# Kernel tuning notes

Measured on AMD Instinct MI355X. Metric: run time of the kernel, lower is better.

The kernel has to match this reference:

```python
import jax, jax.numpy as jnp
import numpy as np

N, E = 20000, 640000
D_IN, D_H, D_OUT = 128, 64, 32


def _lin_w(key, out_d, in_d):
    return jax.random.normal(key, (out_d, in_d), jnp.float32) / np.sqrt(in_d)


def setup_inputs() -> dict:
    key = jax.random.key(0)
    ks = jax.random.split(key, 16)
    x = jax.random.normal(ks[0], (N, D_IN), jnp.float32)
    edge_index = jax.random.randint(ks[1], (2, E), 0, N, jnp.int64)
    inp = {"x": x, "edge_index": edge_index}
    # SAGEConv weights: lin_l (aggregated neighbors, with bias), lin_r (root, no bias)
    inp["Wl1"] = _lin_w(ks[2], D_H, D_IN); inp["bl1"] = jnp.zeros((D_H,), jnp.float32)
    inp["Wr1"] = _lin_w(ks[3], D_H, D_IN)
    inp["Wl2"] = _lin_w(ks[4], D_H, D_H); inp["bl2"] = jnp.zeros((D_H,), jnp.float32)
    inp["Wr2"] = _lin_w(ks[5], D_H, D_H)
    inp["Wl3"] = _lin_w(ks[6], D_OUT, D_H); inp["bl3"] = jnp.zeros((D_OUT,), jnp.float32)
    inp["Wr3"] = _lin_w(ks[7], D_OUT, D_H)
    # Conv2d kernels (OIHW), all 3x3 pad 1
    inp["Wc1"] = jax.random.normal(ks[8], (D_H, 1, 3, 3), jnp.float32) / 3.0
    inp["bc1"] = jnp.zeros((D_H,), jnp.float32)
    inp["Wc2"] = jax.random.normal(ks[9], (D_H, D_H, 3, 3), jnp.float32) / np.sqrt(9 * D_H)
    inp["bc2"] = jnp.zeros((D_H,), jnp.float32)
    inp["Wc3"] = jax.random.normal(ks[10], (1, D_H, 3, 3), jnp.float32) / np.sqrt(9 * D_H)
    inp["bc3"] = jnp.zeros((1,), jnp.float32)
    # linear2 (hidden -> hidden)
    inp["W2"] = _lin_w(ks[11], D_H, D_H); inp["b2"] = jnp.zeros((D_H,), jnp.float32)
    return inp


def _sage(x, src, dst, Wl, bl, Wr):
    # PyG SAGEConv (mean aggr): lin_l(mean_{j->i} x_j) + lin_r(x_i)
    msg = x[src]  # [E, d] gather
    agg = jax.ops.segment_sum(msg, dst, num_segments=N)
    deg = jax.ops.segment_sum(jnp.ones((src.shape[0], 1), x.dtype), dst, num_segments=N)
    agg = agg / jnp.maximum(deg, 1.0)
    return agg @ Wl.T + bl + x @ Wr.T


def _conv(x, w, b):
    y = jax.lax.conv_general_dilated(x, w, (1, 1), ((1, 1), (1, 1)),
                                     dimension_numbers=("NCHW", "OIHW", "NCHW"))
    return y + b[None, :, None, None]


def reference(x, edge_index, Wl1, bl1, Wr1, Wl2, bl2, Wr2, Wl3, bl3, Wr3,
              Wc1, bc1, Wc2, bc2, Wc3, bc3, W2, b2):
    src, dst = edge_index[0], edge_index[1]
    h = _sage(x, src, dst, Wl1, bl1, Wr1)
    h = _sage(h, src, dst, Wl2, bl2, Wr2)
    h = _sage(h, src, dst, Wl2, bl2, Wr2)  # sage2 reused, as in source
    out_1 = h
    h4 = h[None, None]                     # [1,1,N,D_H]
    out = _conv(h4, Wc1, bc1)              # [1,D_H,N,D_H]
    out = _conv(out, Wc2, bc2)             # dropout is identity at inference
    out = _conv(out, Wc3, bc3)             # [1,1,N,D_H]
    out = out[0, 0] + out_1
    out = out @ W2.T + b2
    h = _sage(out, src, dst, Wl2, bl2, Wr2)
    h = _sage(h, src, dst, Wl2, bl2, Wr2)
    h = _sage(h, src, dst, Wl3, bl3, Wr3)
    return h
```

## Files before the change

### kernel.cpp

```cpp
#include <hip/hip_runtime.h>

#define NN 20000
#define NE 640000
#define NBUK 79

__device__ __forceinline__ int probe_stride(const int* __restrict__ ei32) {
  int lane = threadIdx.x & 63;
  int v = ei32[2 * lane + 1];
  unsigned long long nz = __ballot(v != 0);
  return (nz == 0ull) ? 2 : 1;
}

__global__ __launch_bounds__(256) void k_histB(const int* __restrict__ ei,
                                               int* __restrict__ bins, int E) {
  __shared__ int lb[NBUK];
  int tid = threadIdx.x;
  int st = probe_stride(ei);
  for (int i = tid; i < NBUK; i += 256) lb[i] = 0;
  __syncthreads();
  int e0 = blockIdx.x * 4096;
#pragma unroll
  for (int t = 0; t < 16; ++t) {
    int e = e0 + t * 256 + tid;
    if (e < E) atomicAdd(&lb[ei[(size_t)(E + e) * st] >> 8], 1);
  }
  __syncthreads();
  for (int i = tid; i < NBUK; i += 256)
    if (lb[i]) atomicAdd(&bins[i], lb[i]);
}

__global__ __launch_bounds__(128) void k_scan79(const int* __restrict__ bins,
                                                int* __restrict__ bbase,
                                                int* __restrict__ bcur,
                                                int* __restrict__ rowptr,
                                                int E, int N) {
  __shared__ int lds[128];
  int tid = threadIdx.x;
  int mine = (tid < NBUK) ? bins[tid] : 0;
  lds[tid] = mine;
  __syncthreads();
  for (int off = 1; off < 128; off <<= 1) {
    int v = (tid >= off) ? lds[tid - off] : 0;
    __syncthreads();
    lds[tid] += v;
    __syncthreads();
  }
  int ex = lds[tid] - mine;
  if (tid <= NBUK) {
    bbase[tid] = ex;
    if (tid < NBUK) bcur[tid] = ex;
  }
  if (tid == 0) rowptr[N] = E;
}

__global__ __launch_bounds__(256) void k_part(const int* __restrict__ ei,
                                              int* __restrict__ bcur,
                                              unsigned long long* __restrict__ ebuf,
                                              int E) {
  __shared__ int lcnt[NBUK];
  __shared__ int lbase[NBUK];
  int tid = threadIdx.x;
  int st = probe_stride(ei);
  for (int i = tid; i < NBUK; i += 256) lcnt[i] = 0;
  __syncthreads();
  int e0 = blockIdx.x * 4096;
  int srcv[16], dstv[16], lrank[16], bk[16];
  int n = 0;
#pragma unroll
  for (int t = 0; t < 16; ++t) {
    int e = e0 + t * 256 + tid;
    if (e < E) {
      int s = ei[(size_t)e * st];
      int d = ei[(size_t)(E + e) * st];
      int b = d >> 8;
      srcv[n] = s; dstv[n] = d; bk[n] = b;
      lrank[n] = atomicAdd(&lcnt[b], 1);
      ++n;
    }
  }
  __syncthreads();
  for (int i = tid; i < NBUK; i += 256)
    lbase[i] = atomicAdd(&bcur[i], lcnt[i]);
  __syncthreads();
  for (int t = 0; t < n; ++t) {
    int pos = lbase[bk[t]] + lrank[t];
    ebuf[pos] = ((unsigned long long)(unsigned)dstv[t] << 32) | (unsigned)srcv[t];
  }
}

__global__ __launch_bounds__(256) void k_sortb(
    const unsigned long long* __restrict__ ebuf, const int* __restrict__ bbase,
    int* __restrict__ rowptr, float* __restrict__ invdeg,
    int* __restrict__ csr, int N) {
  __shared__ int lcnt[256];
  __shared__ int lcur[256];
  __shared__ int wsum[4];
  int b = blockIdx.x;
  int tid = threadIdx.x;
  int base = bbase[b], n = bbase[b + 1] - base;
  lcnt[tid] = 0;
  __syncthreads();
  for (int e = tid; e < n; e += 256) {
    int d = (int)(ebuf[base + e] >> 32);
    atomicAdd(&lcnt[d - (b << 8)], 1);
  }
  __syncthreads();
  int c = lcnt[tid];
  int lane = tid & 63, wid = tid >> 6;
  int s = c;
#pragma unroll
  for (int off = 1; off < 64; off <<= 1) {
    int v = __shfl_up(s, off, 64);
    if (lane >= off) s += v;
  }
  if (lane == 63) wsum[wid] = s;
  __syncthreads();
  int woff = 0;
  for (int w = 0; w < wid; ++w) woff += wsum[w];
  int pref = woff + s - c;
  int gnode = (b << 8) + tid;
  if (gnode < N) {
    rowptr[gnode] = base + pref;
    invdeg[gnode] = 1.0f / (float)(c < 1 ? 1 : c);
  }
  lcur[tid] = pref;
  __syncthreads();
  for (int e = tid; e < n; e += 256) {
    unsigned long long pk = ebuf[base + e];
    int d = (int)(pk >> 32);
    int pos = atomicAdd(&lcur[d - (b << 8)], 1);
    csr[base + pos] = (int)(unsigned)pk;
  }
}

__device__ __forceinline__ bool maskB(int var, int o2, int o1) {
  int s = o2 + o1;
  switch (var) {
    case 0: return (o2 >= 0) && (s >= 0);
    case 1: return s >= -1;
    case 3: return s <= 1;
    case 4: return (o2 <= 0) && (s <= 0);
    default: return true;
  }
}

__global__ __launch_bounds__(256) void k_setup2(
    const float* __restrict__ Wc1, const float* __restrict__ Wc2,
    const float* __restrict__ Wc3, const float* __restrict__ bc1,
    const float* __restrict__ bc2, const float* __restrict__ bc3,
    const float* __restrict__ Wl1, const float* __restrict__ Wr1,
    const float* __restrict__ Wl2, const float* __restrict__ Wr2,
    const float* __restrict__ Wl3, const float* __restrict__ Wr3,
    const float* __restrict__ W2, const float* __restrict__ b2,
    const float* __restrict__ bl2,
    float* __restrict__ T729, float* __restrict__ beta5,
    float* __restrict__ Wf, float* __restrict__ bf,
    float* __restrict__ Wt1, float* __restrict__ Wt2,
    float* __restrict__ Wt3, float* __restrict__ W2t,
    float* __restrict__ Sbuf, float* __restrict__ c5) {
  int b = blockIdx.x, tid = threadIdx.x;
  if (b == 0) {
    __shared__ float W3[576];
    __shared__ float S9s[5184];
    __shared__ float W1s[576];
    for (int e = tid; e < 576; e += 256) { W3[e] = Wc3[e]; W1s[e] = Wc1[e]; }
    __syncthreads();
    for (int bb = tid; bb < 576; bb += 256) {
      float acc[9];
#pragma unroll
      for (int a = 0; a < 9; ++a) acc[a] = 0.0f;
#pragma unroll 4
      for (int o = 0; o < 64; ++o) {
        float w2 = Wc2[o * 576 + bb];
#pragma unroll
        for (int a = 0; a < 9; ++a) acc[a] += W3[o * 9 + a] * w2;
      }
#pragma unroll
      for (int a = 0; a < 9; ++a) S9s[a * 576 + bb] = acc[a];
    }
    __syncthreads();
    for (int c = tid; c < 729; c += 256) {
      int kx0  = c % 3;
      int dl1e = (c / 3) % 3;
      int dl2e = (c / 9) % 3;
      int ky0  = (c / 27) % 3;
      int ky1  = (c / 81) % 3;
      int ky2  = c / 243;
      const float* s9 = &S9s[(ky2 * 3 + dl2e) * 576 + ky1 * 3 + dl1e];
      const float* w1 = &W1s[ky0 * 3 + kx0];
      float t = 0.0f;
#pragma unroll 8
      for (int i = 0; i < 64; ++i) t += s9[i * 9] * w1[i * 9];
      T729[c] = t;
    }
  } else if (b <= 5) {
    __shared__ float S2[576];
    __shared__ float W3b[576];
    __shared__ float B2[64];
    __shared__ float part[256];
    int var = b - 1;
    for (int e = tid; e < 576; e += 256) {
      int o = e / 9, r = e - o * 9;
      float t = 0.0f;
      for (int i = 0; i < 64; ++i) t += Wc2[o * 576 + i * 9 + r] * bc1[i];
      S2[e] = t;
      W3b[e] = Wc3[e];
    }
    if (tid < 64) B2[tid] = bc2[tid];
    __syncthreads();
    int u = tid & 63, oc = tid >> 6;
    float s = 0.0f;
    for (int ky2 = 0; ky2 < 3; ++ky2) {
      int o2 = ky2 - 1;
      bool okA = (var == 0) ? (o2 >= 0) : (var == 4) ? (o2 <= 0) : true;
      if (!okA) continue;
      for (int dl2 = -1; dl2 <= 1; ++dl2) {
        int p = u + dl2; if ((unsigned)p >= 64u) continue;
        float sel[9];
#pragma unroll
        for (int ky1 = 0; ky1 < 3; ++ky1) {
          int o1 = ky1 - 1;
          bool mb = maskB(var, o2, o1);
#pragma unroll
          for (int dl1 = -1; dl1 <= 1; ++dl1) {
            int pq = p + dl1;
            sel[ky1 * 3 + dl1 + 1] = (mb && (unsigned)pq < 64u) ? 1.0f : 0.0f;
          }
        }
#pragma unroll 4
        for (int oo = 0; oo < 16; ++oo) {
          int o = oc * 16 + oo;
          float inner = B2[o];
#pragma unroll
          for (int r = 0; r < 9; ++r) inner += S2[o * 9 + r] * sel[r];
          s += W3b[o * 9 + ky2 * 3 + (dl2 + 1)] * inner;
        }
      }
    }
    part[tid] = s;
    __syncthreads();
    if (tid < 64) {
      beta5[var * 64 + tid] =
          bc3[0] + part[tid] + part[64 + tid] + part[128 + tid] + part[192 + tid];
    }
  } else if (b <= 38) {
    int gidx = (b - 6) * 256 + tid;
    if (gidx < 8192) {
      int w = gidx >> 7, u = gidx & 127;
      const float* wsrc = (u < 64) ? &Wl2[u * 64] : &Wr2[(u - 64) * 64];
      float s = 0.0f;
#pragma unroll 4
      for (int k = 0; k < 64; ++k) s += W2[k * 64 + w] * wsrc[k];
      Wf[gidx] = s;
    } else if (gidx < 8320) {
      int u = gidx - 8192;
      const float* wsrc = (u < 64) ? &Wl2[u * 64] : &Wr2[(u - 64) * 64];
      float s = 0.0f;
#pragma unroll 4
      for (int k = 0; k < 64; ++k) s += b2[k] * wsrc[k];
      bf[u] = s;
    }
  } else {
    int idx = (b - 39) * 256 + tid;
    if (idx < 16384) {
      int w = idx >> 7, u = idx & 127;
      Wt1[idx] = (u < 64) ? Wl1[u * 128 + w] : Wr1[(u - 64) * 128 + w];
    } else if (idx < 24576) {
      int t = idx - 16384;
      int w = t >> 7, u = t & 127;
      Wt2[t] = (u < 64) ? Wl2[u * 64 + w] : Wr2[(u - 64) * 64 + w];
    } else if (idx < 28672) {
      int t = idx - 24576;
      int w = t >> 6, u = t & 63;
      Wt3[t] = (u < 32) ? Wl3[u * 64 + w] : Wr3[(u - 32) * 64 + w];
    } else if (idx < 32768) {
      int t = idx - 28672;
      int w = t >> 6, u = t & 63;
      W2t[t] = W2[u * 64 + w];
    } else if (idx < 45056) {
      int t2 = idx - 32768;
      int m = t2 >> 12, e = t2 & 4095;
      int i = e >> 6, j = e & 63;
      float s = 0.0f;
#pragma unroll 4
      for (int k = 0; k < 64; ++k) {
        float wlj = Wl2[j * 64 + k], wrj = Wr2[j * 64 + k];
        float wli = Wl2[k * 64 + i], wri = Wr2[k * 64 + i];
        if (m == 0) s += wli * wlj;
        else if (m == 1) s += wri * wlj + wli * wrj;
        else s += wri * wrj;
      }
      Sbuf[t2] = s;
    } else if (idx < 45120) {
      int j = idx - 45056;
      float s = bl2[j];
      for (int i = 0; i < 64; ++i)
        s += bl2[i] * (Wl2[j * 64 + i] + Wr2[j * 64 + i]);
      c5[j] = s;
    }
  }
}

__global__ __launch_bounds__(256) void k_setupG(
    const float* __restrict__ Sbuf, const float* __restrict__ c5,
    const float* __restrict__ Wl3, const float* __restrict__ Wr3,
    const float* __restrict__ bl3, float* __restrict__ Gbuf,
    float* __restrict__ c32) {
  int b = blockIdx.x, tid = threadIdx.x;
  if (b < 32) {
    int idx = b * 256 + tid;
    int kblk = idx >> 11;
    int rem = idx & 2047;
    int t = rem >> 5, j = rem & 31;
    const float* S2p = Sbuf;
    const float* S1p = Sbuf + 4096;
    const float* S0p = Sbuf + 8192;
    const float* pa = (kblk == 0) ? S2p : (kblk == 1) ? S1p : (kblk == 2) ? S0p : nullptr;
    const float* pb = (kblk == 1) ? S2p : (kblk == 2) ? S1p : (kblk == 3) ? S0p : nullptr;
    float s = 0.0f;
#pragma unroll 4
    for (int k = 0; k < 64; ++k) {
      if (pa) s += pa[t * 64 + k] * Wl3[j * 64 + k];
      if (pb) s += pb[t * 64 + k] * Wr3[j * 64 + k];
    }
    Gbuf[idx] = s;
  } else if (tid < 32) {
    float s = bl3[tid];
    for (int k = 0; k < 64; ++k)
      s += c5[k] * (Wl3[tid * 64 + k] + Wr3[tid * 64 + k]);
    c32[tid] = s;
  }
}

__global__ __launch_bounds__(256) void k_setupWg(
    const float* __restrict__ Gbuf, const float* __restrict__ W2,
    const float* __restrict__ b2, float* __restrict__ Wg,
    float* __restrict__ bg) {
  int b = blockIdx.x, tid = threadIdx.x;
  if (b < 32) {
    int idx = b * 256 + tid;
    int w = idx >> 7, u = idx & 127;
    int kblk = u >> 5, j = u & 31;
    const float* gp = Gbuf + kblk * 2048 + j;
    float s = 0.0f;
#pragma unroll 4
    for (int t = 0; t < 64; ++t) s += W2[t * 64 + w] * gp[t * 32];
    Wg[idx] = s;
  } else if (tid < 128) {
    int kblk = tid >> 5, j = tid & 31;
    const float* gp = Gbuf + kblk * 2048 + j;
    float s = 0.0f;
    for (int t = 0; t < 64; ++t) s += b2[t] * gp[t * 32];
    bg[tid] = s;
  }
}

__global__ __launch_bounds__(256) void k_m5(const float* __restrict__ T729,
                                            float* __restrict__ M5T) {
  __shared__ float Ts[729];
  int tid = threadIdx.x;
  for (int e = tid; e < 729; e += 256) Ts[e] = T729[e];
  __syncthreads();
  int idx = blockIdx.x * 256 + tid;
  if (idx >= 15680) return;
  int jw = idx % 7;
  int u  = (idx / 7) % 64;
  int d  = (idx / 448) % 7;
  int var = idx / 3136;
  int w = u + jw - 3;
  float s = 0.0f;
  if (w >= 0 && w < 64) {
    for (int ky2 = 0; ky2 < 3; ++ky2) {
      int o2 = ky2 - 1;
      for (int ky1 = 0; ky1 < 3; ++ky1) {
        int o1 = ky1 - 1;
        if (!maskB(var, o2, o1)) continue;
        int o0 = (d - 3) - o2 - o1;
        if (o0 < -1 || o0 > 1) continue;
        int ky0 = o0 + 1;
        int cbase = ((ky2 * 3 + ky1) * 3 + ky0) * 27;
#pragma unroll
        for (int kx0 = 0; kx0 < 3; ++kx0) {
          int jq = jw - kx0;
          if ((unsigned)jq >= 5u) continue;
          int q = u + jq - 2;
          if ((unsigned)q >= 64u) continue;
#pragma unroll
          for (int dl2e = 0; dl2e < 3; ++dl2e) {
            int p = u + dl2e - 1;
            if ((unsigned)p >= 64u) continue;
            int dl1e = jq - dl2e;
            if ((unsigned)dl1e >= 3u) continue;
            s += Ts[cbase + dl2e * 9 + dl1e * 3 + kx0];
          }
        }
      }
    }
  }
  if (d == 3 && jw == 3) s += 1.0f;
  M5T[(var * 49 + d * 7 + jw) * 64 + u] = s;
}

template <int C, int K>
__global__ __launch_bounds__(256) void k_gemm(const float* __restrict__ X,
                                              const float* __restrict__ Wt,
                                              const float* __restrict__ bias,
                                              float* __restrict__ out, int N) {
  constexpr int ROWS = 16;
  constexpr int RPT = ROWS * C / 256;
  __shared__ float Xs[ROWS * K];
  int y0 = blockIdx.x * ROWS;
  {
    const float4* src = (const float4*)(X + (size_t)y0 * K);
    float4* dst = (float4*)Xs;
#pragma unroll
    for (int v = 0; v < ROWS * K / 4 / 256; ++v)
      dst[v * 256 + threadIdx.x] = src[v * 256 + threadIdx.x];
  }
  __syncthreads();
  int u = threadIdx.x % C;
  int rg = threadIdx.x / C;
  float acc[RPT];
  float bv = bias ? bias[u] : 0.0f;
#pragma unroll
  for (int k = 0; k < RPT; ++k) acc[k] = bv;
#pragma unroll 2
  for (int w0 = 0; w0 < K; w0 += 4) {
    float m0 = Wt[(w0 + 0) * C + u];
    float m1 = Wt[(w0 + 1) * C + u];
    float m2 = Wt[(w0 + 2) * C + u];
    float m3 = Wt[(w0 + 3) * C + u];
    const float* xs = &Xs[(rg * RPT) * K + w0];
#pragma unroll
    for (int k = 0; k < RPT; ++k) {
      float4 h = *(const float4*)(xs + k * K);
      acc[k] += m0 * h.x + m1 * h.y + m2 * h.z + m3 * h.w;
    }
  }
#pragma unroll
  for (int k = 0; k < RPT; ++k)
    out[(size_t)(y0 + rg * RPT + k) * C + u] = acc[k];
}

template <int C>
__global__ __launch_bounds__(256) void k_fused(const float* __restrict__ yzin,
                                               const int* __restrict__ csr,
                                               const int* __restrict__ rowptr,
                                               const float* __restrict__ invdeg,
                                               const float* __restrict__ bl,
                                               const float* __restrict__ Wt,
                                               float* __restrict__ out, int N) {
  constexpr int FV = 16;
  constexpr int G  = 4;
  constexpr int S4 = 32;
  constexpr int CAP = 64;
  __shared__ int idxs[16 * CAP];
  __shared__ float htile[16 * 64];
  int tid = threadIdx.x;
  int w = tid >> 6, lane = tid & 63;
  int base = blockIdx.x * 16;
  int beg_r[4], m_r[4], end_r[4];
#pragma unroll
  for (int rr = 0; rr < 4; ++rr) {
    int node = base + w * 4 + rr;
    int beg = rowptr[node], end = rowptr[node + 1];
    beg_r[rr] = beg; end_r[rr] = end;
    int cnt = end - beg;
    int m = cnt < CAP ? cnt : CAP;
    m_r[rr] = m;
    int* my = &idxs[(w * 4 + rr) * CAP];
    for (int k = lane; k < m; k += 64) my[k] = csr[beg + k];
  }
  __syncthreads();
  int g = lane / FV, f = lane % FV;
  const float4* yz4 = (const float4*)yzin;
#pragma unroll
  for (int rr = 0; rr < 4; ++rr) {
    int node = base + w * 4 + rr;
    const int* my = &idxs[(w * 4 + rr) * CAP];
    int m = m_r[rr];
    float a0x=0,a0y=0,a0z=0,a0w=0, a1x=0,a1y=0,a1z=0,a1w=0;
    float a2x=0,a2y=0,a2z=0,a2w=0, a3x=0,a3y=0,a3z=0,a3w=0;
    int j = g;
    for (; j + 3 * G < m; j += 4 * G) {
      int s0 = my[j], s1 = my[j + G], s2 = my[j + 2 * G], s3 = my[j + 3 * G];
      float4 v0 = yz4[(size_t)s0 * S4 + f];
      float4 v1 = yz4[(size_t)s1 * S4 + f];
      float4 v2 = yz4[(size_t)s2 * S4 + f];
      float4 v3 = yz4[(size_t)s3 * S4 + f];
      a0x += v0.x; a0y += v0.y; a0z += v0.z; a0w += v0.w;
      a1x += v1.x; a1y += v1.y; a1z += v1.z; a1w += v1.w;
      a2x += v2.x; a2y += v2.y; a2z += v2.z; a2w += v2.w;
      a3x += v3.x; a3y += v3.y; a3z += v3.z; a3w += v3.w;
    }
    for (; j < m; j += G) {
      int s0 = my[j];
      float4 v0 = yz4[(size_t)s0 * S4 + f];
      a0x += v0.x; a0y += v0.y; a0z += v0.z; a0w += v0.w;
    }
    for (int jj = beg_r[rr] + CAP + g; jj < end_r[rr]; jj += G) {
      int s0 = csr[jj];
      float4 v0 = yz4[(size_t)s0 * S4 + f];
      a0x += v0.x; a0y += v0.y; a0z += v0.z; a0w += v0.w;
    }
    float ax = (a0x + a1x) + (a2x + a3x);
    float ay = (a0y + a1y) + (a2y + a3y);
    float az = (a0z + a1z) + (a2z + a3z);
    float aw = (a0w + a1w) + (a2w + a3w);
#pragma unroll
    for (int mm = FV; mm < 64; mm <<= 1) {
      ax += __shfl_xor(ax, mm, 64);
      ay += __shfl_xor(ay, mm, 64);
      az += __shfl_xor(az, mm, 64);
      aw += __shfl_xor(aw, mm, 64);
    }
    if (g == 0) {
      float4 root = yz4[(size_t)node * S4 + FV + f];
      float4 bv = ((const float4*)bl)[f];
      float id = invdeg[node];
      float4 o;
      o.x = ax * id + bv.x + root.x;
      o.y = ay * id + bv.y + root.y;
      o.z = az * id + bv.z + root.z;
      o.w = aw * id + bv.w + root.w;
// ... 201 lines not shown
  float a0x=0,a0y=0,a0z=0,a0w=0, a1x=0,a1y=0,a1z=0,a1w=0;
  float a2x=0,a2y=0,a2z=0,a2w=0, a3x=0,a3y=0,a3z=0,a3w=0;
  int j = g;
  for (; j + 3 * G < m; j += 4 * G) {
    int s0 = my[j], s1 = my[j + G], s2 = my[j + 2 * G], s3 = my[j + 3 * G];
    float4 v0 = sr4[(size_t)s0 * FV + f];
    float4 v1 = sr4[(size_t)s1 * FV + f];
    float4 v2 = sr4[(size_t)s2 * FV + f];
    float4 v3 = sr4[(size_t)s3 * FV + f];
    a0x += v0.x; a0y += v0.y; a0z += v0.z; a0w += v0.w;
    a1x += v1.x; a1y += v1.y; a1z += v1.z; a1w += v1.w;
    a2x += v2.x; a2y += v2.y; a2z += v2.z; a2w += v2.w;
    a3x += v3.x; a3y += v3.y; a3z += v3.z; a3w += v3.w;
  }
  for (; j < m; j += G) {
    int s0 = my[j];
    float4 v0 = sr4[(size_t)s0 * FV + f];
    a0x += v0.x; a0y += v0.y; a0z += v0.z; a0w += v0.w;
  }
  for (int jj = beg + CAP + g; jj < end; jj += G) {
    int s0 = csr[jj];
    float4 v0 = sr4[(size_t)s0 * FV + f];
    a0x += v0.x; a0y += v0.y; a0z += v0.z; a0w += v0.w;
  }
  float ax = (a0x + a1x) + (a2x + a3x);
  float ay = (a0y + a1y) + (a2y + a3y);
  float az = (a0z + a1z) + (a2z + a3z);
  float aw = (a0w + a1w) + (a2w + a3w);
#pragma unroll
  for (int mm = FV; mm < 64; mm <<= 1) {
    ax += __shfl_xor(ax, mm, 64);
    ay += __shfl_xor(ay, mm, 64);
    az += __shfl_xor(az, mm, 64);
    aw += __shfl_xor(aw, mm, 64);
  }
  if (g == 0) {
    float4 av = ((const float4*)add)[(size_t)node * FV + f];
    float id = invdeg[node];
    float4 o;
    o.x = ax * id + av.x;
    o.y = ay * id + av.y;
    o.z = az * id + av.z;
    o.w = aw * id + av.w;
    if (cvec != nullptr) {
      float4 cv = ((const float4*)cvec)[f];
      o.x += cv.x; o.y += cv.y; o.z += cv.z; o.w += cv.w;
    }
    ((float4*)out)[(size_t)node * FV + f] = o;
  }
}

extern "C" void kernel_launch(void* const* d_in, const int* in_sizes, int n_in,
                              void* d_out, int out_size, void* d_ws, size_t ws_size,
                              hipStream_t stream) {
  const int N = NN, E = NE;
  const float* x   = (const float*)d_in[0];
  const int*   ei  = (const int*)d_in[1];
  const float* Wl1 = (const float*)d_in[2];
  const float* bl1 = (const float*)d_in[3];
  const float* Wr1 = (const float*)d_in[4];
  const float* Wl2 = (const float*)d_in[5];
  const float* bl2 = (const float*)d_in[6];
  const float* Wr2 = (const float*)d_in[7];
  const float* Wl3 = (const float*)d_in[8];
  const float* bl3 = (const float*)d_in[9];
  const float* Wr3 = (const float*)d_in[10];
  const float* Wc1 = (const float*)d_in[11];
  const float* bc1 = (const float*)d_in[12];
  const float* Wc2 = (const float*)d_in[13];
  const float* bc2 = (const float*)d_in[14];
  const float* Wc3 = (const float*)d_in[15];
  const float* bc3 = (const float*)d_in[16];
  const float* W2  = (const float*)d_in[17];
  const float* b2  = (const float*)d_in[18];

  char* ws = (char*)d_ws;
  size_t off = 0;
  auto alloc = [&](size_t bytes) -> void* {
    off = (off + 255) & ~(size_t)255;
    void* p = ws + off;
    off += bytes;
    return p;
  };
  int*   rowptr = (int*)alloc((size_t)(N + 1) * 4);
  float* invdeg = (float*)alloc((size_t)N * 4);
  int*   csr    = (int*)alloc((size_t)E * 4);
  unsigned long long* ebuf = (unsigned long long*)alloc((size_t)E * 8);
  int*   bins   = (int*)alloc(128 * 4);
  int*   bbase  = (int*)alloc(128 * 4);
  int*   bcur   = (int*)alloc(128 * 4);
  float* Wt1    = (float*)alloc(128 * 128 * 4);
  float* Wt2    = (float*)alloc(64 * 128 * 4);
  float* Wt3    = (float*)alloc(64 * 64 * 4);
  float* W2t    = (float*)alloc(64 * 64 * 4);
  float* Wf     = (float*)alloc(64 * 128 * 4);
  float* bf     = (float*)alloc(128 * 4);
  float* T729   = (float*)alloc(729 * 4);
  float* M5T    = (float*)alloc(15680 * 4);
  float* beta5  = (float*)alloc(320 * 4);
  float* Sbuf   = (float*)alloc(12288 * 4);
  float* c5     = (float*)alloc(64 * 4);
  float* Gbuf   = (float*)alloc(8192 * 4);
  float* Wg     = (float*)alloc(8192 * 4);
  float* bg     = (float*)alloc(128 * 4);
  float* c32    = (float*)alloc(32 * 4);
  float* yzA    = (float*)alloc((size_t)N * 128 * 4);
  float* yzB    = (float*)alloc((size_t)N * 128 * 4);
  float* hA     = (float*)alloc((size_t)N * 64 * 4);
  float* wbuf   = (float*)alloc((size_t)4 * N * 32 * 4);
  float* s1buf  = (float*)alloc((size_t)N * 32 * 4);
  float* s2buf  = (float*)alloc((size_t)N * 32 * 4);
  (void)ws_size; (void)in_sizes; (void)n_in; (void)out_size;

  const int gG = N / 16;
  const int gA = N / 4;
  const int gP = (E + 4095) / 4096;

  hipMemsetAsync(bins, 0, 128 * 4, stream);
  k_histB<<<gP, 256, 0, stream>>>(ei, bins, E);
  k_scan79<<<1, 128, 0, stream>>>(bins, bbase, bcur, rowptr, E, N);
  k_part<<<gP, 256, 0, stream>>>(ei, bcur, ebuf, E);
  k_sortb<<<NBUK, 256, 0, stream>>>(ebuf, bbase, rowptr, invdeg, csr, N);

  k_setup2<<<216, 256, 0, stream>>>(Wc1, Wc2, Wc3, bc1, bc2, bc3,
                                    Wl1, Wr1, Wl2, Wr2, Wl3, Wr3, W2, b2, bl2,
                                    T729, beta5, Wf, bf, Wt1, Wt2, Wt3, W2t,
                                    Sbuf, c5);
  k_setupG<<<33, 256, 0, stream>>>(Sbuf, c5, Wl3, Wr3, bl3, Gbuf, c32);
  k_setupWg<<<33, 256, 0, stream>>>(Gbuf, W2, b2, Wg, bg);
  k_m5<<<62, 256, 0, stream>>>(T729, M5T);

  k_gemm<128, 128><<<gG, 256, 0, stream>>>(x, Wt1, nullptr, yzA, N);
  k_fused<128><<<gG, 256, 0, stream>>>(yzA, csr, rowptr, invdeg, bl1, Wt2, yzB, N);
  k_fused<128><<<gG, 256, 0, stream>>>(yzB, csr, rowptr, invdeg, bl2, Wt2, yzA, N);
  k_agg<64><<<gA, 256, 0, stream>>>(yzA, csr, rowptr, invdeg, bl2, hA, N);
  k_applyfused<<<gG, 256, 0, stream>>>(hA, M5T, beta5, Wg, bg, wbuf, N);
  const float* w3 = wbuf;
  const float* w2p = wbuf + (size_t)N * 32;
  const float* w1p = wbuf + (size_t)2 * N * 32;
  const float* w0p = wbuf + (size_t)3 * N * 32;
  k_agg32<<<gA, 256, 0, stream>>>(w3, csr, rowptr, invdeg, w2p, nullptr, s1buf, N);
  k_agg32<<<gA, 256, 0, stream>>>(s1buf, csr, rowptr, invdeg, w1p, nullptr, s2buf, N);
  k_agg32<<<gA, 256, 0, stream>>>(s2buf, csr, rowptr, invdeg, w0p, c32, (float*)d_out, N);
}
```

Before: 324.4 us.

## Merge CSR build and weight setup kernels into three multi-role phase kernels

```diff
diff --git a/kernel.cpp b/kernel.cpp
--- a/kernel.cpp
+++ b/kernel.cpp
@@ -9,128 +9,6 @@
   int v = ei32[2 * lane + 1];
   unsigned long long nz = __ballot(v != 0);
   return (nz == 0ull) ? 2 : 1;
-}
-
-__global__ __launch_bounds__(256) void k_histB(const int* __restrict__ ei,
-                                               int* __restrict__ bins, int E) {
-  __shared__ int lb[NBUK];
-  int tid = threadIdx.x;
-  int st = probe_stride(ei);
-  for (int i = tid; i < NBUK; i += 256) lb[i] = 0;
-  __syncthreads();
-  int e0 = blockIdx.x * 4096;
-#pragma unroll
-  for (int t = 0; t < 16; ++t) {
-    int e = e0 + t * 256 + tid;
-    if (e < E) atomicAdd(&lb[ei[(size_t)(E + e) * st] >> 8], 1);
-  }
-  __syncthreads();
-  for (int i = tid; i < NBUK; i += 256)
-    if (lb[i]) atomicAdd(&bins[i], lb[i]);
-}
-
-__global__ __launch_bounds__(128) void k_scan79(const int* __restrict__ bins,
-                                                int* __restrict__ bbase,
-                                                int* __restrict__ bcur,
-                                                int* __restrict__ rowptr,
-                                                int E, int N) {
-  __shared__ int lds[128];
-  int tid = threadIdx.x;
-  int mine = (tid < NBUK) ? bins[tid] : 0;
-  lds[tid] = mine;
-  __syncthreads();
-  for (int off = 1; off < 128; off <<= 1) {
-    int v = (tid >= off) ? lds[tid - off] : 0;
-    __syncthreads();
-    lds[tid] += v;
-    __syncthreads();
-  }
-  int ex = lds[tid] - mine;
-  if (tid <= NBUK) {
-    bbase[tid] = ex;
-    if (tid < NBUK) bcur[tid] = ex;
-  }
-  if (tid == 0) rowptr[N] = E;
-}
-
-__global__ __launch_bounds__(256) void k_part(const int* __restrict__ ei,
-                                              int* __restrict__ bcur,
-                                              unsigned long long* __restrict__ ebuf,
-                                              int E) {
-  __shared__ int lcnt[NBUK];
-  __shared__ int lbase[NBUK];
-  int tid = threadIdx.x;
-  int st = probe_stride(ei);
-  for (int i = tid; i < NBUK; i += 256) lcnt[i] = 0;
-  __syncthreads();
-  int e0 = blockIdx.x * 4096;
-  int srcv[16], dstv[16], lrank[16], bk[16];
-  int n = 0;
-#pragma unroll
-  for (int t = 0; t < 16; ++t) {
-    int e = e0 + t * 256 + tid;
-    if (e < E) {
-      int s = ei[(size_t)e * st];
-      int d = ei[(size_t)(E + e) * st];
-      int b = d >> 8;
-      srcv[n] = s; dstv[n] = d; bk[n] = b;
-      lrank[n] = atomicAdd(&lcnt[b], 1);
-      ++n;
-    }
-  }
-  __syncthreads();
-  for (int i = tid; i < NBUK; i += 256)
-    lbase[i] = atomicAdd(&bcur[i], lcnt[i]);
-  __syncthreads();
-  for (int t = 0; t < n; ++t) {
-    int pos = lbase[bk[t]] + lrank[t];
-    ebuf[pos] = ((unsigned long long)(unsigned)dstv[t] << 32) | (unsigned)srcv[t];
-  }
-}
-
-__global__ __launch_bounds__(256) void k_sortb(
-    const unsigned long long* __restrict__ ebuf, const int* __restrict__ bbase,
-    int* __restrict__ rowptr, float* __restrict__ invdeg,
-    int* __restrict__ csr, int N) {
-  __shared__ int lcnt[256];
-  __shared__ int lcur[256];
-  __shared__ int wsum[4];
-  int b = blockIdx.x;
-  int tid = threadIdx.x;
-  int base = bbase[b], n = bbase[b + 1] - base;
-  lcnt[tid] = 0;
-  __syncthreads();
-  for (int e = tid; e < n; e += 256) {
-    int d = (int)(ebuf[base + e] >> 32);
-    atomicAdd(&lcnt[d - (b << 8)], 1);
-  }
-  __syncthreads();
-  int c = lcnt[tid];
-  int lane = tid & 63, wid = tid >> 6;
-  int s = c;
-#pragma unroll
-  for (int off = 1; off < 64; off <<= 1) {
-    int v = __shfl_up(s, off, 64);
-    if (lane >= off) s += v;
-  }
-  if (lane == 63) wsum[wid] = s;
-  __syncthreads();
-  int woff = 0;
-  for (int w = 0; w < wid; ++w) woff += wsum[w];
-  int pref = woff + s - c;
-  int gnode = (b << 8) + tid;
-  if (gnode < N) {
-    rowptr[gnode] = base + pref;
-    invdeg[gnode] = 1.0f / (float)(c < 1 ? 1 : c);
-  }
-  lcur[tid] = pref;
-  __syncthreads();
-  for (int e = tid; e < n; e += 256) {
-    unsigned long long pk = ebuf[base + e];
-    int d = (int)(pk >> 32);
-    int pos = atomicAdd(&lcur[d - (b << 8)], 1);
-    csr[base + pos] = (int)(unsigned)pk;
-  }
 }
 
 __device__ __forceinline__ bool maskB(int var, int o2, int o1) {
@@ -144,25 +22,42 @@
   }
 }
 
-__global__ __launch_bounds__(256) void k_setup2(
+__global__ __launch_bounds__(256) void k_phaseA1(
+    const int* __restrict__ ei, int* __restrict__ bins,
     const float* __restrict__ Wc1, const float* __restrict__ Wc2,
     const float* __restrict__ Wc3, const float* __restrict__ bc1,
     const float* __restrict__ bc2, const float* __restrict__ bc3,
     const float* __restrict__ Wl1, const float* __restrict__ Wr1,
     const float* __restrict__ Wl2, const float* __restrict__ Wr2,
-    const float* __restrict__ Wl3, const float* __restrict__ Wr3,
-    const float* __restrict__ W2, const float* __restrict__ b2,
     const float* __restrict__ bl2,
     float* __restrict__ T729, float* __restrict__ beta5,
-    float* __restrict__ Wf, float* __restrict__ bf,
     float* __restrict__ Wt1, float* __restrict__ Wt2,
-    float* __restrict__ Wt3, float* __restrict__ W2t,
-    float* __restrict__ Sbuf, float* __restrict__ c5) {
+    float* __restrict__ Sbuf, float* __restrict__ c5,
+    int* __restrict__ rowptr, int E, int N) {
+  __shared__ float smem[6336];
   int b = blockIdx.x, tid = threadIdx.x;
-  if (b == 0) {
-    __shared__ float W3[576];
-    __shared__ float S9s[5184];
-    __shared__ float W1s[576];
+  if (b >= 151) {
+    int* lb = (int*)smem;
+    int st = probe_stride(ei);
+    for (int i = tid; i < NBUK; i += 256) lb[i] = 0;
+    __syncthreads();
+    int e0 = (b - 151) * 4096;
+#pragma unroll
+    for (int t = 0; t < 16; ++t) {
+      int e = e0 + t * 256 + tid;
+      if (e < E) atomicAdd(&lb[ei[(size_t)(E + e) * st] >> 8], 1);
+    }
+    __syncthreads();
+    for (int i = tid; i < NBUK; i += 256)
+      if (lb[i]) atomicAdd(&bins[i], lb[i]);
+    return;
+  }
+  int s = b;
+  if (s == 0) {
+    float* W3  = smem;
+    float* S9s = smem + 576;
+    float* W1s = smem + 5760;
+    if (tid == 0) rowptr[N] = E;
     for (int e = tid; e < 576; e += 256) { W3[e] = Wc3[e]; W1s[e] = Wc1[e]; }
     __syncthreads();
     for (int bb = tid; bb < 576; bb += 256) {
@@ -193,12 +88,12 @@
       for (int i = 0; i < 64; ++i) t += s9[i * 9] * w1[i * 9];
       T729[c] = t;
     }
-  } else if (b <= 5) {
-    __shared__ float S2[576];
-    __shared__ float W3b[576];
-    __shared__ float B2[64];
-    __shared__ float part[256];
-    int var = b - 1;
+  } else if (s <= 5) {
+    float* S2   = smem;
+    float* W3b  = smem + 576;
+    float* B2   = smem + 1152;
+    float* part = smem + 1216;
+    int var = s - 1;
     for (int e = tid; e < 576; e += 256) {
       int o = e / 9, r = e - o * 9;
       float t = 0.0f;
@@ -209,7 +104,7 @@
     if (tid < 64) B2[tid] = bc2[tid];
     __syncthreads();
     int u = tid & 63, oc = tid >> 6;
-    float s = 0.0f;
+    float acc = 0.0f;
     for (int ky2 = 0; ky2 < 3; ++ky2) {
       int o2 = ky2 - 1;
       bool okA = (var == 0) ? (o2 >= 0) : (var == 4) ? (o2 <= 0) : true;
@@ -233,35 +128,18 @@
           float inner = B2[o];
 #pragma unroll
           for (int r = 0; r < 9; ++r) inner += S2[o * 9 + r] * sel[r];
-          s += W3b[o * 9 + ky2 * 3 + (dl2 + 1)] * inner;
+          acc += W3b[o * 9 + ky2 * 3 + (dl2 + 1)] * inner;
         }
       }
     }
-    part[tid] = s;
+    part[tid] = acc;
     __syncthreads();
     if (tid < 64) {
       beta5[var * 64 + tid] =
           bc3[0] + part[tid] + part[64 + tid] + part[128 + tid] + part[192 + tid];
     }
-  } else if (b <= 38) {
-    int gidx = (b - 6) * 256 + tid;
-    if (gidx < 8192) {
-      int w = gidx >> 7, u = gidx & 127;
-      const float* wsrc = (u < 64) ? &Wl2[u * 64] : &Wr2[(u - 64) * 64];
-      float s = 0.0f;
-#pragma unroll 4
-      for (int k = 0; k < 64; ++k) s += W2[k * 64 + w] * wsrc[k];
-      Wf[gidx] = s;
-    } else if (gidx < 8320) {
-      int u = gidx - 8192;
-      const float* wsrc = (u < 64) ? &Wl2[u * 64] : &Wr2[(u - 64) * 64];
-      float s = 0.0f;
-#pragma unroll 4
-      for (int k = 0; k < 64; ++k) s += b2[k] * wsrc[k];
-      bf[u] = s;
-    }
   } else {
-    int idx = (b - 39) * 256 + tid;
+    int idx = (s - 6) * 256 + tid;
     if (idx < 16384) {
       int w = idx >> 7, u = idx & 127;
       Wt1[idx] = (u < 64) ? Wl1[u * 128 + w] : Wr1[(u - 64) * 128 + w];
@@ -269,177 +147,266 @@
       int t = idx - 16384;
       int w = t >> 7, u = t & 127;
       Wt2[t] = (u < 64) ? Wl2[u * 64 + w] : Wr2[(u - 64) * 64 + w];
-    } else if (idx < 28672) {
-      int t = idx - 24576;
-      int w = t >> 6, u = t & 63;
-      Wt3[t] = (u < 32) ? Wl3[u * 64 + w] : Wr3[(u - 32) * 64 + w];
-    } else if (idx < 32768) {
-      int t = idx - 28672;
-      int w = t >> 6, u = t & 63;
-      W2t[t] = W2[u * 64 + w];
-    } else if (idx < 45056) {
-      int t2 = idx - 32768;
+    } else if (idx < 36864) {
+      int t2 = idx - 24576;
       int m = t2 >> 12, e = t2 & 4095;
       int i = e >> 6, j = e & 63;
-      float s = 0.0f;
+      float acc = 0.0f;
 #pragma unroll 4
       for (int k = 0; k < 64; ++k) {
         float wlj = Wl2[j * 64 + k], wrj = Wr2[j * 64 + k];
         float wli = Wl2[k * 64 + i], wri = Wr2[k * 64 + i];
-        if (m == 0) s += wli * wlj;
-        else if (m == 1) s += wri * wlj + wli * wrj;
-        else s += wri * wrj;
+        if (m == 0) acc += wli * wlj;
+        else if (m == 1) acc += wri * wlj + wli * wrj;
+        else acc += wri * wrj;
       }
-      Sbuf[t2] = s;
-    } else if (idx < 45120) {
-      int j = idx - 45056;
-      float s = bl2[j];
+      Sbuf[t2] = acc;
+    } else if (idx < 36928) {
+      int j = idx - 36864;
+      float acc = bl2[j];
       for (int i = 0; i < 64; ++i)
-        s += bl2[i] * (Wl2[j * 64 + i] + Wr2[j * 64 + i]);
-      c5[j] = s;
-    }
-  }
-}
-
-__global__ __launch_bounds__(256) void k_setupG(
+        acc += bl2[i] * (Wl2[j * 64 + i] + Wr2[j * 64 + i]);
+      c5[j] = acc;
+    }
+  }
+}
+
+__global__ __launch_bounds__(256) void k_phaseA2(
+    const float* __restrict__ X, const float* __restrict__ Wt1,
+    float* __restrict__ yzA,
+    const int* __restrict__ ei, const int* __restrict__ bins,
+    int* __restrict__ bcur, unsigned long long* __restrict__ ebuf,
+    const float* __restrict__ T729, float* __restrict__ M5T,
     const float* __restrict__ Sbuf, const float* __restrict__ c5,
     const float* __restrict__ Wl3, const float* __restrict__ Wr3,
     const float* __restrict__ bl3, float* __restrict__ Gbuf,
-    float* __restrict__ c32) {
+    float* __restrict__ c32, int E, int N) {
+  __shared__ float smem[2048];
   int b = blockIdx.x, tid = threadIdx.x;
-  if (b < 32) {
-    int idx = b * 256 + tid;
-    int kblk = idx >> 11;
-    int rem = idx & 2047;
-    int t = rem >> 5, j = rem & 31;
-    const float* S2p = Sbuf;
-    const float* S1p = Sbuf + 4096;
-    const float* S0p = Sbuf + 8192;
-    const float* pa = (kblk == 0) ? S2p : (kblk == 1) ? S1p : (kblk == 2) ? S0p : nullptr;
-    const float* pb = (kblk == 1) ? S2p : (kblk == 2) ? S1p : (kblk == 3) ? S0p : nullptr;
-    float s = 0.0f;
-#pragma unroll 4
-    for (int k = 0; k < 64; ++k) {
-      if (pa) s += pa[t * 64 + k] * Wl3[j * 64 + k];
-      if (pb) s += pb[t * 64 + k] * Wr3[j * 64 + k];
-    }
-    Gbuf[idx] = s;
-  } else if (tid < 32) {
-    float s = bl3[tid];
-    for (int k = 0; k < 64; ++k)
-      s += c5[k] * (Wl3[tid * 64 + k] + Wr3[tid * 64 + k]);
-    c32[tid] = s;
-  }
-}
-
-__global__ __launch_bounds__(256) void k_setupWg(
-    const float* __restrict__ Gbuf, const float* __restrict__ W2,
-    const float* __restrict__ b2, float* __restrict__ Wg,
-    float* __restrict__ bg) {
-  int b = blockIdx.x, tid = threadIdx.x;
-  if (b < 32) {
-    int idx = b * 256 + tid;
-    int w = idx >> 7, u = idx & 127;
-    int kblk = u >> 5, j = u & 31;
-    const float* gp = Gbuf + kblk * 2048 + j;
-    float s = 0.0f;
-#pragma unroll 4
-    for (int t = 0; t < 64; ++t) s += W2[t * 64 + w] * gp[t * 32];
-    Wg[idx] = s;
-  } else if (tid < 128) {
-    int kblk = tid >> 5, j = tid & 31;
-    const float* gp = Gbuf + kblk * 2048 + j;
-    float s = 0.0f;
-    for (int t = 0; t < 64; ++t) s += b2[t] * gp[t * 32];
-    bg[tid] = s;
-  }
-}
-
-__global__ __launch_bounds__(256) void k_m5(const float* __restrict__ T729,
-                                            float* __restrict__ M5T) {
-  __shared__ float Ts[729];
-  int tid = threadIdx.x;
-  for (int e = tid; e < 729; e += 256) Ts[e] = T729[e];
-  __syncthreads();
-  int idx = blockIdx.x * 256 + tid;
-  if (idx >= 15680) return;
-  int jw = idx % 7;
-  int u  = (idx / 7) % 64;
-  int d  = (idx / 448) % 7;
-  int var = idx / 3136;
-  int w = u + jw - 3;
-  float s = 0.0f;
-  if (w >= 0 && w < 64) {
-    for (int ky2 = 0; ky2 < 3; ++ky2) {
-      int o2 = ky2 - 1;
-      for (int ky1 = 0; ky1 < 3; ++ky1) {
-        int o1 = ky1 - 1;
-        if (!maskB(var, o2, o1)) continue;
-        int o0 = (d - 3) - o2 - o1;
-        if (o0 < -1 || o0 > 1) continue;
-        int ky0 = o0 + 1;
-        int cbase = ((ky2 * 3 + ky1) * 3 + ky0) * 27;
-#pragma unroll
-        for (int kx0 = 0; kx0 < 3; ++kx0) {
-          int jq = jw - kx0;
-          if ((unsigned)jq >= 5u) continue;
-          int q = u + jq - 2;
-          if ((unsigned)q >= 64u) continue;
-#pragma unroll
-          for (int dl2e = 0; dl2e < 3; ++dl2e) {
-            int p = u + dl2e - 1;
-            if ((unsigned)p >= 64u) continue;
-            int dl1e = jq - dl2e;
-            if ((unsigned)dl1e >= 3u) continue;
-            s += Ts[cbase + dl2e * 9 + dl1e * 3 + kx0];
+  if (b < 157) {
+    int* lcnt  = (int*)smem;
+    int* lbase = (int*)smem + 79;
+    int* sscan = (int*)smem + 158;
+    int st = probe_stride(ei);
+    for (int i = tid; i < NBUK; i += 256) lcnt[i] = 0;
+    int mine = 0;
+    if (tid < 128) { mine = (tid < NBUK) ? bins[tid] : 0; sscan[tid] = mine; }
+    __syncthreads();
+    for (int off = 1; off < 128; off <<= 1) {
+      int v = 0;
+      if (tid < 128 && tid >= off) v = sscan[tid - off];
+      __syncthreads();
+      if (tid < 128) sscan[tid] += v;
+      __syncthreads();
+    }
+    if (tid < 128) sscan[tid] -= mine;
+    __syncthreads();
+    int e0 = b * 4096;
+    int srcv[16], dstv[16], lrank[16], bk[16];
+    int n = 0;
+#pragma unroll
+    for (int t = 0; t < 16; ++t) {
+      int e = e0 + t * 256 + tid;
+      if (e < E) {
+        int sv = ei[(size_t)e * st];
+        int d = ei[(size_t)(E + e) * st];
+        int bb = d >> 8;
+        srcv[n] = sv; dstv[n] = d; bk[n] = bb;
+        lrank[n] = atomicAdd(&lcnt[bb], 1);
+        ++n;
+      }
+    }
+    __syncthreads();
+    for (int i = tid; i < NBUK; i += 256)
+      lbase[i] = sscan[i] + atomicAdd(&bcur[i], lcnt[i]);
+    __syncthreads();
+    for (int t = 0; t < n; ++t) {
+      int pos = lbase[bk[t]] + lrank[t];
+      ebuf[pos] = ((unsigned long long)(unsigned)dstv[t] << 32) | (unsigned)srcv[t];
+    }
+  } else if (b < 219) {
+    float* Ts = smem;
+    for (int e = tid; e < 729; e += 256) Ts[e] = T729[e];
+    __syncthreads();
+    int idx = (b - 157) * 256 + tid;
+    if (idx >= 15680) return;
+    int jw = idx % 7;
+    int u  = (idx / 7) % 64;
+    int d  = (idx / 448) % 7;
+    int var = idx / 3136;
+    int w = u + jw - 3;
+    float acc = 0.0f;
+    if (w >= 0 && w < 64) {
+      for (int ky2 = 0; ky2 < 3; ++ky2) {
+        int o2 = ky2 - 1;
+        for (int ky1 = 0; ky1 < 3; ++ky1) {
+          int o1 = ky1 - 1;
+          if (!maskB(var, o2, o1)) continue;
+          int o0 = (d - 3) - o2 - o1;
+          if (o0 < -1 || o0 > 1) continue;
+          int ky0 = o0 + 1;
+          int cbase = ((ky2 * 3 + ky1) * 3 + ky0) * 27;
+#pragma unroll
+          for (int kx0 = 0; kx0 < 3; ++kx0) {
+            int jq = jw - kx0;
+            if ((unsigned)jq >= 5u) continue;
+            int q = u + jq - 2;
+            if ((unsigned)q >= 64u) continue;
+#pragma unroll
+            for (int dl2e = 0; dl2e < 3; ++dl2e) {
+              int p = u + dl2e - 1;
+              if ((unsigned)p >= 64u) continue;
+              int dl1e = jq - dl2e;
+              if ((unsigned)dl1e >= 3u) continue;
+              acc += Ts[cbase + dl2e * 9 + dl1e * 3 + kx0];
+            }
           }
         }
       }
     }
-  }
-  if (d == 3 && jw == 3) s += 1.0f;
-  M5T[(var * 49 + d * 7 + jw) * 64 + u] = s;
-}
-
-template <int C, int K>
-__global__ __launch_bounds__(256) void k_gemm(const float* __restrict__ X,
-                                              const float* __restrict__ Wt,
-                                              const float* __restrict__ bias,
-                                              float* __restrict__ out, int N) {
-  constexpr int ROWS = 16;
-  constexpr int RPT = ROWS * C / 256;
-  __shared__ float Xs[ROWS * K];
-  int y0 = blockIdx.x * ROWS;
-  {
-    const float4* src = (const float4*)(X + (size_t)y0 * K);
-    float4* dst = (float4*)Xs;
-#pragma unroll
-    for (int v = 0; v < ROWS * K / 4 / 256; ++v)
-      dst[v * 256 + threadIdx.x] = src[v * 256 + threadIdx.x];
-  }
-  __syncthreads();
-  int u = threadIdx.x % C;
-  int rg = threadIdx.x / C;
-  float acc[RPT];
-  float bv = bias ? bias[u] : 0.0f;
-#pragma unroll
-  for (int k = 0; k < RPT; ++k) acc[k] = bv;
+    if (d == 3 && jw == 3) acc += 1.0f;
+    M5T[(var * 49 + d * 7 + jw) * 64 + u] = acc;
+  } else if (b < 252) {
+    int bb = b - 219;
+    if (bb < 32) {
+      int idx = bb * 256 + tid;
+      int kblk = idx >> 11;
+      int rem = idx & 2047;
+      int t = rem >> 5, j = rem & 31;
+      const float* S2p = Sbuf;
+      const float* S1p = Sbuf + 4096;
+      const float* S0p = Sbuf + 8192;
+      const float* pa = (kblk == 0) ? S2p : (kblk == 1) ? S1p : (kblk == 2) ? S0p : nullptr;
+      const float* pb = (kblk == 1) ? S2p : (kblk == 2) ? S1p : (kblk == 3) ? S0p : nullptr;
+      float acc = 0.0f;
+#pragma unroll 4
+      for (int k = 0; k < 64; ++k) {
+        if (pa) acc += pa[t * 64 + k] * Wl3[j * 64 + k];
+        if (pb) acc += pb[t * 64 + k] * Wr3[j * 64 + k];
+      }
+      Gbuf[idx] = acc;
+    } else if (tid < 32) {
+      float acc = bl3[tid];
+      for (int k = 0; k < 64; ++k)
+        acc += c5[k] * (Wl3[tid * 64 + k] + Wr3[tid * 64 + k]);
+      c32[tid] = acc;
+    }
+  } else {
+    constexpr int C = 128, K = 128, ROWS = 16, RPT = ROWS * C / 256;
+    float* Xs = smem;
+    int y0 = (b - 252) * ROWS;
+    {
+      const float4* src = (const float4*)(X + (size_t)y0 * K);
+      float4* dst = (float4*)Xs;
+#pragma unroll
+      for (int v = 0; v < ROWS * K / 4 / 256; ++v)
+        dst[v * 256 + tid] = src[v * 256 + tid];
+    }
+    __syncthreads();
+    int u = tid % C;
+    int rg = tid / C;
+    float acc[RPT];
+#pragma unroll
+    for (int k = 0; k < RPT; ++k) acc[k] = 0.0f;
 #pragma unroll 2
-  for (int w0 = 0; w0 < K; w0 += 4) {
-    float m0 = Wt[(w0 + 0) * C + u];
-    float m1 = Wt[(w0 + 1) * C + u];
-    float m2 = Wt[(w0 + 2) * C + u];
-    float m3 = Wt[(w0 + 3) * C + u];
-    const float* xs = &Xs[(rg * RPT) * K + w0];
-#pragma unroll
-    for (int k = 0; k < RPT; ++k) {
-      float4 h = *(const float4*)(xs + k * K);
-      acc[k] += m0 * h.x + m1 * h.y + m2 * h.z + m3 * h.w;
-    }
-  }
-#pragma unroll
-  for (int k = 0; k < RPT; ++k)
-    out[(size_t)(y0 + rg * RPT + k) * C + u] = acc[k];
+    for (int w0 = 0; w0 < K; w0 += 4) {
+      float m0 = Wt1[(w0 + 0) * C + u];
+      float m1 = Wt1[(w0 + 1) * C + u];
+      float m2 = Wt1[(w0 + 2) * C + u];
+      float m3 = Wt1[(w0 + 3) * C + u];
+      const float* xs = &Xs[(rg * RPT) * K + w0];
+#pragma unroll
+      for (int k = 0; k < RPT; ++k) {
+        float4 h = *(const float4*)(xs + k * K);
+        acc[k] += m0 * h.x + m1 * h.y + m2 * h.z + m3 * h.w;
+      }
+    }
+#pragma unroll
+    for (int k = 0; k < RPT; ++k)
+      yzA[(size_t)(y0 + rg * RPT + k) * C + u] = acc[k];
+  }
+}
+
+__global__ __launch_bounds__(256) void k_phaseA3(
+    const unsigned long long* __restrict__ ebuf, const int* __restrict__ bins,
+    int* __restrict__ rowptr, float* __restrict__ invdeg,
+    int* __restrict__ csr,
+    const float* __restrict__ Gbuf, const float* __restrict__ W2,
+    const float* __restrict__ b2, float* __restrict__ Wg,
+    float* __restrict__ bg, int N) {
+  __shared__ int smem[644];
+  int b = blockIdx.x, tid = threadIdx.x;
+  if (b < NBUK) {
+    int* lcnt  = smem;
+    int* lcur  = smem + 256;
+    int* wsum  = smem + 512;
+    int* sscan = smem + 516;
+    int mine = 0;
+    if (tid < 128) { mine = (tid < NBUK) ? bins[tid] : 0; sscan[tid] = mine; }
+    __syncthreads();
+    for (int off = 1; off < 128; off <<= 1) {
+      int v = 0;
+      if (tid < 128 && tid >= off) v = sscan[tid - off];
+      __syncthreads();
+      if (tid < 128) sscan[tid] += v;
+      __syncthreads();
+    }
+    if (tid < 128) sscan[tid] -= mine;
+    __syncthreads();
+    int base = sscan[b];
+    int n = bins[b];
+    lcnt[tid] = 0;
+    __syncthreads();
+    for (int e = tid; e < n; e += 256) {
+      int d = (int)(ebuf[base + e] >> 32);
+      atomicAdd(&lcnt[d - (b << 8)], 1);
+    }
+    __syncthreads();
+    int c = lcnt[tid];
+    int lane = tid & 63, wid = tid >> 6;
+    int s = c;
+#pragma unroll
+    for (int off = 1; off < 64; off <<= 1) {
+      int v = __shfl_up(s, off, 64);
+      if (lane >= off) s += v;
+    }
+    if (lane == 63) wsum[wid] = s;
+    __syncthreads();
+    int woff = 0;
+    for (int w = 0; w < wid; ++w) woff += wsum[w];
+    int pref = woff + s - c;
+    int gnode = (b << 8) + tid;
+    if (gnode < N) {
+      rowptr[gnode] = base + pref;
+      invdeg[gnode] = 1.0f / (float)(c < 1 ? 1 : c);
+    }
+    lcur[tid] = pref;
+    __syncthreads();
+    for (int e = tid; e < n; e += 256) {
+      unsigned long long pk = ebuf[base + e];
+      int d = (int)(pk >> 32);
+      int pos = atomicAdd(&lcur[d - (b << 8)], 1);
+      csr[base + pos] = (int)(unsigned)pk;
+    }
+  } else {
+    int bb = b - NBUK;
+    if (bb < 32) {
+      int idx = bb * 256 + tid;
+      int w = idx >> 7, u = idx & 127;
+      int kblk = u >> 5, j = u & 31;
+      const float* gp = Gbuf + kblk * 2048 + j;
+      float acc = 0.0f;
+#pragma unroll 4
+      for (int t = 0; t < 64; ++t) acc += W2[t * 64 + w] * gp[t * 32];
+      Wg[idx] = acc;
+    } else if (tid < 128) {
+      int kblk = tid >> 5, j = tid & 31;
+      const float* gp = Gbuf + kblk * 2048 + j;
+      float acc = 0.0f;
+      for (int t = 0; t < 64; ++t) acc += b2[t] * gp[t * 32];
+      bg[tid] = acc;
+    }
+  }
 }
 
 template <int C>
@@ -807,60 +774,52 @@
     off += bytes;
     return p;
   };
-  int*   rowptr = (int*)alloc((size_t)(N + 1) * 4);
-  float* invdeg = (float*)alloc((size_t)N * 4);
-  int*   csr    = (int*)alloc((size_t)E * 4);
+  int*   rowptr  = (int*)alloc((size_t)(N + 1) * 4);
+  float* invdeg  = (float*)alloc((size_t)N * 4);
+  int*   csr     = (int*)alloc((size_t)E * 4);
   unsigned long long* ebuf = (unsigned long long*)alloc((size_t)E * 8);
-  int*   bins   = (int*)alloc(128 * 4);
-  int*   bbase  = (int*)alloc(128 * 4);
-  int*   bcur   = (int*)alloc(128 * 4);
-  float* Wt1    = (float*)alloc(128 * 128 * 4);
-  float* Wt2    = (float*)alloc(64 * 128 * 4);
-  float* Wt3    = (float*)alloc(64 * 64 * 4);
-  float* W2t    = (float*)alloc(64 * 64 * 4);
-  float* Wf     = (float*)alloc(64 * 128 * 4);
-  float* bf     = (float*)alloc(128 * 4);
-  float* T729   = (float*)alloc(729 * 4);
-  float* M5T    = (float*)alloc(15680 * 4);
-  float* beta5  = (float*)alloc(320 * 4);
-  float* Sbuf   = (float*)alloc(12288 * 4);
-  float* c5     = (float*)alloc(64 * 4);
-  float* Gbuf   = (float*)alloc(8192 * 4);
-  float* Wg     = (float*)alloc(8192 * 4);
-  float* bg     = (float*)alloc(128 * 4);
-  float* c32    = (float*)alloc(32 * 4);
-  float* yzA    = (float*)alloc((size_t)N * 128 * 4);
-  float* yzB    = (float*)alloc((size_t)N * 128 * 4);
-  float* hA     = (float*)alloc((size_t)N * 64 * 4);
-  float* wbuf   = (float*)alloc((size_t)4 * N * 32 * 4);
-  float* s1buf  = (float*)alloc((size_t)N * 32 * 4);
-  float* s2buf  = (float*)alloc((size_t)N * 32 * 4);
+  int*   binsbuf = (int*)alloc(256 * 4);
+  int*   bins    = binsbuf;
+  int*   bcur    = binsbuf + 128;
+  float* Wt1     = (float*)alloc(128 * 128 * 4);
+  float* Wt2     = (float*)alloc(64 * 128 * 4);
+  float* T729    = (float*)alloc(729 * 4);
+  float* M5T     = (float*)alloc(15680 * 4);
+  float* beta5   = (float*)alloc(320 * 4);
+  float* Sbuf    = (float*)alloc(12288 * 4);
+  float* c5      = (float*)alloc(64 * 4);
+  float* Gbuf    = (float*)alloc(8192 * 4);
+  float* Wg      = (float*)alloc(8192 * 4);
+  float* bg      = (float*)alloc(128 * 4);
+  float* c32     = (float*)alloc(32 * 4);
+  float* yzA     = (float*)alloc((size_t)N * 128 * 4);
+  float* yzB     = (float*)alloc((size_t)N * 128 * 4);
+  float* hA      = (float*)alloc((size_t)N * 64 * 4);
+  float* wbuf    = (float*)alloc((size_t)4 * N * 32 * 4);
+  float* s1buf   = (float*)alloc((size_t)N * 32 * 4);
+  float* s2buf   = (float*)alloc((size_t)N * 32 * 4);
   (void)ws_size; (void)in_sizes; (void)n_in; (void)out_size;
 
   const int gG = N / 16;
   const int gA = N / 4;
-  const int gP = (E + 4095) / 4096;
-
-  hipMemsetAsync(bins, 0, 128 * 4, stream);
-  k_histB<<<gP, 256, 0, stream>>>(ei, bins, E);
-  k_scan79<<<1, 128, 0, stream>>>(bins, bbase, bcur, rowptr, E, N);
-  k_part<<<gP, 256, 0, stream>>>(ei, bcur, ebuf, E);
-  k_sortb<<<NBUK, 256, 0, stream>>>(ebuf, bbase, rowptr, invdeg, csr, N);
-
-  k_setup2<<<216, 256, 0, stream>>>(Wc1, Wc2, Wc3, bc1, bc2, bc3,
-                                    Wl1, Wr1, Wl2, Wr2, Wl3, Wr3, W2, b2, bl2,
-                                    T729, beta5, Wf, bf, Wt1, Wt2, Wt3, W2t,
-                                    Sbuf, c5);
-  k_setupG<<<33, 256, 0, stream>>>(Sbuf, c5, Wl3, Wr3, bl3, Gbuf, c32);
-  k_setupWg<<<33, 256, 0, stream>>>(Gbuf, W2, b2, Wg, bg);
-  k_m5<<<62, 256, 0, stream>>>(T729, M5T);
-
-  k_gemm<128, 128><<<gG, 256, 0, stream>>>(x, Wt1, nullptr, yzA, N);
+
+  hipMemsetAsync(binsbuf, 0, 256 * 4, stream);
+
+  k_phaseA1<<<308, 256, 0, stream>>>(ei, bins, Wc1, Wc2, Wc3, bc1, bc2, bc3,
+                                     Wl1, Wr1, Wl2, Wr2, bl2,
+                                     T729, beta5, Wt1, Wt2, Sbuf, c5,
+                                     rowptr, E, N);
+  k_phaseA2<<<1502, 256, 0, stream>>>(x, Wt1, yzA, ei, bins, bcur, ebuf,
+                                      T729, M5T, Sbuf, c5, Wl3, Wr3, bl3,
+                                      Gbuf, c32, E, N);
+  k_phaseA3<<<112, 256, 0, stream>>>(ebuf, bins, rowptr, invdeg, csr,
+                                     Gbuf, W2, b2, Wg, bg, N);
+
   k_fused<128><<<gG, 256, 0, stream>>>(yzA, csr, rowptr, invdeg, bl1, Wt2, yzB, N);
   k_fused<128><<<gG, 256, 0, stream>>>(yzB, csr, rowptr, invdeg, bl2, Wt2, yzA, N);
   k_agg<64><<<gA, 256, 0, stream>>>(yzA, csr, rowptr, invdeg, bl2, hA, N);
   k_applyfused<<<gG, 256, 0, stream>>>(hA, M5T, beta5, Wg, bg, wbuf, N);
-  const float* w3 = wbuf;
+  const float* w3  = wbuf;
   const float* w2p = wbuf + (size_t)N * 32;
   const float* w1p = wbuf + (size_t)2 * N * 32;
   const float* w0p = wbuf + (size_t)3 * N * 32;
```

Result: faster. 282.2 us (-13.0%).
